# Kernel optimization log

Hardware: AMD Instinct MI355X
Metric: run time of the kernel (lower is better)

## Reference

```python
import jax, jax.numpy as jnp
import numpy as np

SELECT_NUM = 5
N_OBJ = 256


def conv(x, w, b, stride=1, pad=None):
    """NCHW conv. pad=None -> VALID; pad=1 -> [(1,1),(1,1)]."""
    padding = 'VALID' if pad is None else [(pad, pad), (pad, pad)]
    out = jax.lax.conv_general_dilated(
        x, w, (stride, stride), padding,
        dimension_numbers=('NCHW', 'OIHW', 'NCHW'))
    return out + b[None, :, None, None]


def setup_inputs() -> dict:
    key = jax.random.key(0)
    ks = jax.random.split(key, 20)

    def p(k, shape, fan_in):
        return (jax.random.normal(k, shape, jnp.float32) / np.float32(np.sqrt(fan_in)))

    inp = {}
    inp['glob_feature'] = jax.random.normal(ks[0], (1, 1024, 28, 28), jnp.float32)
    inp['roi_features'] = jax.random.normal(ks[1], (N_OBJ, 2048, 7, 7), jnp.float32)
    # valid boxes in a 1280x720 image: x1>x0, y1>y0 so log(.) is finite
    x0 = jax.random.uniform(ks[2], (N_OBJ,), minval=0.0, maxval=600.0)
    y0 = jax.random.uniform(ks[3], (N_OBJ,), minval=0.0, maxval=340.0)
    x1 = x0 + jax.random.uniform(ks[4], (N_OBJ,), minval=10.0, maxval=600.0)
    y1 = y0 + jax.random.uniform(ks[5], (N_OBJ,), minval=10.0, maxval=340.0)
    inp['bbox'] = jnp.stack([x0, y0, x1, y1], axis=1)

    # global branch
    inp['w_glob1'] = p(ks[6], (512, 1024, 4, 4), 1024 * 16); inp['b_glob1'] = jnp.zeros(512, jnp.float32)
    inp['w_glob2'] = p(ks[7], (256, 512, 4, 4), 512 * 16);   inp['b_glob2'] = jnp.zeros(256, jnp.float32)
    # object branch
    inp['w_obj1'] = p(ks[8], (1024, 2048, 3, 3), 2048 * 9);  inp['b_obj1'] = jnp.zeros(1024, jnp.float32)
    inp['w_obj2'] = p(ks[9], (256, 1024, 3, 3), 1024 * 9);   inp['b_obj2'] = jnp.zeros(256, jnp.float32)
    # selector (516 = 260 obj + 256 glob)
    inp['w_sel1'] = p(ks[10], (256, 516, 3, 3), 516 * 9);    inp['b_sel1'] = jnp.zeros(256, jnp.float32)
    inp['w_sel2'] = p(ks[11], (16, 256, 3, 3), 256 * 9);     inp['b_sel2'] = jnp.zeros(16, jnp.float32)
    inp['w_sel3'] = p(ks[12], (1, 16, 3, 3), 16 * 9);        inp['b_sel3'] = jnp.zeros(1, jnp.float32)
    # FC head (eval mode: dropout = identity)
    inp['w_fc1'] = p(ks[13], (516, 256), 516);               inp['b_fc1'] = jnp.zeros(256, jnp.float32)
    inp['w_fc2'] = p(ks[14], (256 * SELECT_NUM, 64), 1280);  inp['b_fc2'] = jnp.zeros(64, jnp.float32)
    inp['w_fc3'] = p(ks[15], (64, 4), 64);                   inp['b_fc3'] = jnp.zeros(4, jnp.float32)
    return inp


def reference(glob_feature, roi_features, bbox,
              w_glob1, b_glob1, w_glob2, b_glob2,
              w_obj1, b_obj1, w_obj2, b_obj2,
              w_sel1, b_sel1, w_sel2, b_sel2, w_sel3, b_sel3,
              w_fc1, b_fc1, w_fc2, b_fc2, w_fc3, b_fc3):
    # global branch: [1,1024,28,28] -> [1,512,14,14] -> [1,256,7,7]; pool(7) is identity
    glob = jax.nn.relu(conv(glob_feature, w_glob1, b_glob1, stride=2, pad=1))
    glob = jax.nn.relu(conv(glob, w_glob2, b_glob2, stride=2, pad=1))

    # object branch: [N,2048,7,7] -> [N,1024,7,7] -> [N,256,7,7]
    obj = jax.nn.relu(conv(roi_features, w_obj1, b_obj1, pad=1))
    obj = jax.nn.relu(conv(obj, w_obj2, b_obj2, pad=1))

    # bbox normalization (uses original coords; image is 1280x720)
    x0, y0, x1, y1 = bbox[:, 0], bbox[:, 1], bbox[:, 2], bbox[:, 3]
    bb = jnp.stack([x0 / 1280.0, y0 / 720.0,
                    jnp.log(1280.0 / (x1 - x0)),
                    jnp.log(720.0 / (y1 - y0))], axis=1)  # [N,4]
    bb = jnp.broadcast_to(bb[:, :, None, None], (bb.shape[0], 4, 7, 7))
    obj = jnp.concatenate([bb, obj], axis=1)  # [N,260,7,7]

    # selector: concat with broadcast glob, 3 valid convs 7->5->3->1
    glob2 = jnp.broadcast_to(glob, (obj.shape[0], 256, 7, 7))
    s = jnp.concatenate([obj, glob2], axis=1)  # [N,516,7,7]
    s = jax.nn.relu(conv(s, w_sel1, b_sel1))
    s = jax.nn.relu(conv(s, w_sel2, b_sel2))
    s = conv(s, w_sel3, b_sel3).reshape(-1)  # [N]

    # top-k selection (sort descending over objects)
    idx = jnp.argsort(-s)[:SELECT_NUM]
    obj = obj[idx] / np.float32(SELECT_NUM)  # [5,260,7,7]

    # adaptive avg pool to 1x1 == mean over HW
    obj = obj.mean(axis=(2, 3))                               # [5,260]
    g = jnp.broadcast_to(glob.mean(axis=(2, 3)), (SELECT_NUM, 256))  # [5,256]
    x = jnp.concatenate([obj, g], axis=1)                     # [5,516]

    x = jax.nn.relu(x @ w_fc1 + b_fc1)   # dropout is identity in eval
    tmp = x.reshape(-1)                  # [1280]
    x = jax.nn.relu(tmp @ w_fc2 + b_fc2) # [64]
    x = x @ w_fc3 + b_fc3                # [4]
    return x
```

## Files before the change

kernel.cpp:

```cpp
#include <hip/hip_runtime.h>
#include <math.h>

using half8 = __attribute__((ext_vector_type(8))) _Float16;
using half4 = __attribute__((ext_vector_type(4))) _Float16;
using f32x4 = __attribute__((ext_vector_type(4))) float;

template<int CIN, int KC, int M_, int BM>
__global__ __launch_bounds__(256)
void transform_w(const float* __restrict__ w, _Float16* __restrict__ wt) {
  constexpr int NT = (KC / 32) * 9;
  __shared__ float lds[32 * 289];
  const int tid = threadIdx.x;
  const int s   = blockIdx.x;
  const int m0  = blockIdx.y * 32;
  const int ci0 = s * 32;
  int vlen = (CIN - ci0) * 9;
  if (vlen > 288) vlen = 288;
  if (vlen < 0) vlen = 0;

  for (int e = tid; e < 32 * 288; e += 256) {
    const int mi = e / 288, o = e - mi * 288;
    float v = 0.f;
    if (o < vlen) v = w[(size_t)(m0 + mi) * (CIN * 9) + (size_t)ci0 * 9 + o];
    lds[mi * 289 + o] = v;
  }
  __syncthreads();

  const int cc  = s >> 2;
  const int sub = s & 3;
  int ns = (KC - 128 * cc) / 32; if (ns > 4) ns = 4;
  const int mt = m0 / BM;
  const int mb = m0 - mt * BM;
  _Float16* base = wt + (size_t)mt * NT * (BM * 32);

  for (int u = tid; u < 36 * 256; u += 256) {
    const int chunk  = u >> 8;
    const int within = u & 255;
    const int g = chunk & 3, khkw = chunk >> 2;
    const int mi = within >> 3, i = within & 7;
    const int kt = 36 * cc + khkw * ns + sub;
    const float v = lds[mi * 289 + (8 * g + i) * 9 + khkw];
    base[(size_t)kt * (BM * 32) + g * (BM * 8) + (mb + mi) * 8 + i] = (_Float16)v;
  }
}

__global__ __launch_bounds__(256)
void convert_tr(const float* __restrict__ x, _Float16* __restrict__ xh) {
  __shared__ _Float16 t_s[49][136];
  const int tid   = threadIdx.x;
  const int cbase = blockIdx.x * 128;
  const int obj   = blockIdx.y;
  const float* src = x + (size_t)obj * 2048 * 49 + (size_t)cbase * 49;
  for (int e = tid; e < 128 * 49; e += 256) {
    const int ci = e / 49, pos = e - ci * 49;
    t_s[pos][ci] = (_Float16)src[e];
  }
  __syncthreads();
  _Float16* dst = xh + (size_t)obj * 49 * 2048 + cbase;
  for (int u = tid; u < 49 * 16; u += 256) {
    const int pos = u >> 4, l = u & 15;
    *(half8*)&dst[(size_t)pos * 2048 + l * 8] = *(const half8*)&t_s[pos][l * 8];
  }
}

template<int KC, int M_, int BM, int FN, int OHW, int PAD, bool TIN, int XROW,
         bool TOUT, typename OUT_T, typename IN_T>
__global__ __launch_bounds__(512, 4)
void conv_mfma(const _Float16* __restrict__ Wt, const IN_T* __restrict__ X,
               const float* __restrict__ bias, OUT_T* __restrict__ out,
               int outc, int co_off) {
  constexpr int NT   = (KC / 32) * 9;
  constexpr int OPOS = OHW * OHW;
  constexpr int WM   = BM / 4;
  constexpr int FR   = WM / 16;

  __shared__ alignas(16) _Float16 x_s[2][50][136];

  const int tid  = threadIdx.x;
  const int wid  = tid >> 6;
  const int lane = tid & 63;
  const int g    = lane >> 4;
  const int ln   = lane & 15;
  const int obj  = wid >> 2;
  const int wm   = (wid & 3) * WM;
  const int mt   = blockIdx.x;
  const int op   = blockIdx.y;

  if (tid < 272) x_s[tid / 136][49][tid % 136] = (_Float16)0.f;

  int ohv[FN], owv[FN];
  bool pvv[FN];
#pragma unroll
  for (int f = 0; f < FN; f++) {
    const int pos = ln + 16 * f;
    pvv[f] = pos < OPOS;
    ohv[f] = pos / OHW;
    owv[f] = pos % OHW;
  }

  f32x4 acc[FR][FN];
#pragma unroll
  for (int r = 0; r < FR; r++)
#pragma unroll
    for (int f = 0; f < FN; f++) acc[r][f] = (f32x4){0.f, 0.f, 0.f, 0.f};

  const _Float16* Xh = nullptr;
  if constexpr (TIN) Xh = (const _Float16*)X + (size_t)(2 * op) * 49 * XROW;

  half8 rg[4];
  auto load_chunk = [&](int cbase, int cw) {
    if (cw == 128) {
#pragma unroll
      for (int v = 0; v < 4; v++) {
        const int u = v * 512 + tid;
        if (u < 1568) {
          const int row = u >> 4, l = u & 15;
          const int o = row >= 49 ? 1 : 0, pos = row - 49 * o;
          rg[v] = *(const half8*)(Xh + (size_t)(o * 49 + pos) * XROW + cbase + l * 8);
        }
      }
    } else {
      if (tid < 392) {
        const int row = tid >> 2, l = tid & 3;
        const int o = row >= 49 ? 1 : 0, pos = row - 49 * o;
        rg[0] = *(const half8*)(Xh + (size_t)(o * 49 + pos) * XROW + cbase + l * 8);
      }
    }
  };
  auto write_chunk = [&](int cw) {
    if (cw == 128) {
#pragma unroll
      for (int v = 0; v < 4; v++) {
        const int u = v * 512 + tid;
        if (u < 1568) {
          const int row = u >> 4, l = u & 15;
          const int o = row >= 49 ? 1 : 0, pos = row - 49 * o;
          *(half8*)&x_s[o][pos][l * 8] = rg[v];
        }
      }
    } else {
      if (tid < 392) {
        const int row = tid >> 2, l = tid & 3;
        const int o = row >= 49 ? 1 : 0, pos = row - 49 * o;
        *(half8*)&x_s[o][pos][l * 8] = rg[0];
      }
    }
  };

  const _Float16* ap = Wt + (size_t)mt * NT * (BM * 32) + (g * BM + wm + ln) * 8;
  half8 afn[FR];
#pragma unroll
  for (int r = 0; r < FR; r++) afn[r] = *(const half8*)(ap + r * 128);

  if constexpr (TIN) load_chunk(0, KC < 128 ? KC : 128);

  for (int cbase = 0; cbase < KC; cbase += 128) {
    const int cw = (KC - cbase < 128) ? (KC - cbase) : 128;
    __syncthreads();
    if constexpr (TIN) {
      write_chunk(cw);
      if (cbase + 128 < KC) {
        const int nw = (KC - cbase - 128 < 128) ? (KC - cbase - 128) : 128;
        load_chunk(cbase + 128, nw);
      }
    } else {
      for (int e = tid; e < 2 * cw * 49; e += 512) {
        const int o = e / (cw * 49);
        const int r = e - o * (cw * 49);
        const int ci = r / 49, pos = r - ci * 49;
        const float v = (float)(X[(size_t)(2 * op + o) * KC * 49 + (size_t)cbase * 49 + r]);
        x_s[o][pos][ci] = (_Float16)v;
      }
    }
    __syncthreads();
    const int nsub = cw / 32;
    for (int khkw = 0; khkw < 9; khkw++) {
      const int kh = khkw / 3, kw = khkw - 3 * (khkw / 3);
      int boff[FN];
#pragma unroll
      for (int f = 0; f < FN; f++) {
        const int ih = ohv[f] + kh - PAD;
        const int iw = owv[f] + kw - PAD;
        bool v = pvv[f];
        if (PAD) v = v && ((unsigned)ih < 7u) && ((unsigned)iw < 7u);
        const int row = v ? (ih * 7 + iw) : 49;
        boff[f] = (obj * 50 * 136 + row * 136) * 2;
      }
      for (int sub = 0; sub < nsub; sub++) {
        half8 af[FR];
#pragma unroll
        for (int r = 0; r < FR; r++) af[r] = afn[r];
        ap += BM * 32;
#pragma unroll
        for (int r = 0; r < FR; r++)
          afn[r] = *(const half8*)(ap + r * 128);
        const char* xb = (const char*)(&x_s[0][0][0]) + (sub * 32 + 8 * g) * 2;
#pragma unroll
        for (int f = 0; f < FN; f++) {
          const half8 bf = *(const half8*)(xb + boff[f]);
#pragma unroll
          for (int r = 0; r < FR; r++)
            acc[r][f] = __builtin_amdgcn_mfma_f32_16x16x32_f16(af[r], bf, acc[r][f], 0, 0, 0);
        }
      }
    }
  }

  const int bo = 2 * op + obj;
#pragma unroll
  for (int f = 0; f < FN; f++) {
    const int pos = ln + 16 * f;
    if (pos < OPOS) {
#pragma unroll
      for (int r = 0; r < FR; r++) {
        const int mrow = mt * BM + wm + r * 16 + g * 4;
        if constexpr (TOUT) {
          half4 h;
#pragma unroll
          for (int e = 0; e < 4; e++)
            h[e] = (_Float16)fmaxf(acc[r][f][e] + bias[mrow + e], 0.f);
          *(half4*)&((_Float16*)out)[((size_t)bo * OPOS + pos) * outc + co_off + mrow] = h;
        } else {
#pragma unroll
          for (int e = 0; e < 4; e++) {
            const int m = mrow + e;
            float v = fmaxf(acc[r][f][e] + bias[m], 0.f);
            out[((size_t)bo * outc + co_off + m) * OPOS + pos] = (OUT_T)v;
          }
        }
      }
    }
  }
}

template<int M_, int CIN, int KH, int KW, int H, int W, int OH, int OW,
         int STRIDE, int PAD, int BATCH, int OUTC, int CO_OFF, bool RELU,
         int TM, int TN, int KSPLIT, bool PARTIAL>
__global__ __launch_bounds__(256)
void conv_gemm(const float* __restrict__ A,
               const float* __restrict__ X,
               const float* __restrict__ bias,
               float* __restrict__ out) {
  constexpr int K   = CIN * KH * KW;
  constexpr int N   = BATCH * OH * OW;
  constexpr int BK  = 16;
  constexpr int BM  = 16 * TM;
  constexpr int BN  = 16 * TN;
  constexpr int KCH = K / KSPLIT;

  __shared__ float a_s[BK][BM];
  __shared__ float b_s[BK][BN];

  const int t  = threadIdx.x;
  const int tx = t & 15;
  const int ty = t >> 4;
  const int n0 = blockIdx.x * BN;
  const int m0 = blockIdx.y * BM;
  const int kz = blockIdx.z;

  constexpr int AQ    = TM / 4;
  constexpr int TPR_A = 4 / AQ;
  const int am = t / TPR_A;
  const int ak = (t % TPR_A) * (4 * AQ);

  constexpr int BQ = TN / 4;
  const int bk = t & 15;
  const int bn = (t >> 4) * TN;

  float acc[TM][TN];
#pragma unroll
  for (int i = 0; i < TM; i++)
#pragma unroll
    for (int j = 0; j < TN; j++) acc[i][j] = 0.f;

  for (int k0 = kz * KCH; k0 < (kz + 1) * KCH; k0 += BK) {
    float4 av[AQ];
#pragma unroll
    for (int q = 0; q < AQ; q++) {
      av[q] = make_float4(0.f, 0.f, 0.f, 0.f);
      const int kq = k0 + ak + 4 * q;
      if ((m0 + am) < M_ && kq < K)
        av[q] = *reinterpret_cast<const float4*>(&A[(m0 + am) * K + kq]);
    }
    float bv[TN];
#pragma unroll
    for (int q = 0; q < TN; q++) bv[q] = 0.f;
    {
      const int kk = k0 + bk;
      if (kk < K) {
        const int ci = kk / (KH * KW);
        const int r  = kk - ci * (KH * KW);
        const int kh = r / KW;
        const int kw = r - kh * KW;
#pragma unroll
        for (int q = 0; q < TN; q++) {
          const int n = n0 + bn + q;
          if (n < N) {
            const int b   = n / (OH * OW);
            const int pos = n - b * (OH * OW);
            const int oh  = pos / OW;
            const int ow  = pos - oh * OW;
            const int ih  = oh * STRIDE - PAD + kh;
            const int iw  = ow * STRIDE - PAD + kw;
            if (ih >= 0 && ih < H && iw >= 0 && iw < W)
              bv[q] = X[((b * CIN + ci) * H + ih) * W + iw];
          }
        }
      }
    }
    __syncthreads();
#pragma unroll
    for (int q = 0; q < AQ; q++) {
      const int kq = ak + 4 * q;
      a_s[kq + 0][am] = av[q].x;
      a_s[kq + 1][am] = av[q].y;
      a_s[kq + 2][am] = av[q].z;
      a_s[kq + 3][am] = av[q].w;
    }
#pragma unroll
    for (int q = 0; q < BQ; q++)
      *reinterpret_cast<float4*>(&b_s[bk][bn + 4 * q]) =
          make_float4(bv[4 * q], bv[4 * q + 1], bv[4 * q + 2], bv[4 * q + 3]);
    __syncthreads();
#pragma unroll
    for (int kk2 = 0; kk2 < BK; kk2++) {
      float a[TM], b[TN];
#pragma unroll
      for (int q = 0; q < AQ; q++)
        *reinterpret_cast<float4*>(&a[4 * q]) =
            *reinterpret_cast<const float4*>(&a_s[kk2][ty * TM + 4 * q]);
#pragma unroll
      for (int q = 0; q < BQ; q++)
        *reinterpret_cast<float4*>(&b[4 * q]) =
            *reinterpret_cast<const float4*>(&b_s[kk2][tx * TN + 4 * q]);
#pragma unroll
      for (int i = 0; i < TM; i++)
#pragma unroll
        for (int j = 0; j < TN; j++)
          acc[i][j] = fmaf(a[i], b[j], acc[i][j]);
    }
  }

#pragma unroll
  for (int i = 0; i < TM; i++) {
    const int m = m0 + ty * TM + i;
    if (m < M_) {
#pragma unroll
      for (int j = 0; j < TN; j++) {
        const int n = n0 + tx * TN + j;
        if (n < N) {
          if (PARTIAL) {
            out[((size_t)kz * M_ + m) * N + n] = acc[i][j];
          } else {
            float v = acc[i][j] + bias[m];
            if (RELU) v = fmaxf(v, 0.f);
            const int b   = n / (OH * OW);
            const int pos = n - b * (OH * OW);
            out[(b * OUTC + CO_OFF + m) * (OH * OW) + pos] = v;
          }
        }
      }
    }
  }
}

__global__ void reduce_bias_relu(const float* __restrict__ part,
                                 const float* __restrict__ bias,
                                 float* __restrict__ out, int MN, int N, int KS) {
  const int e = blockIdx.x * 256 + threadIdx.x;
  if (e >= MN) return;
  float s = 0.f;
  for (int k = 0; k < KS; k++) s += part[(size_t)k * MN + e];
  s += bias[e / N];
  out[e] = fmaxf(s, 0.f);
}

__global__ __launch_bounds__(256)
void sel2_kernel(const float* __restrict__ x, const float* __restrict__ w,
                 const float* __restrict__ b, float* __restrict__ out) {
  const int wv   = (blockIdx.x * 256 + threadIdx.x) >> 6;
  const int lane = threadIdx.x & 63;
  const int obj  = wv >> 4, co = wv & 15;
  float acc[9];
#pragma unroll
  for (int p = 0; p < 9; p++) acc[p] = 0.f;
  const float* xo = x + (size_t)obj * 256 * 25;
  const float* wo = w + (size_t)co * 2304;
  for (int k = lane; k < 2304; k += 64) {
    const int ci = k / 9, rr = k - 9 * ci;
    const int kh = rr / 3, kw = rr - 3 * kh;
    const float wval = wo[k];
    const float* xc = xo + ci * 25;
#pragma unroll
    for (int oh = 0; oh < 3; oh++)
#pragma unroll
      for (int ow = 0; ow < 3; ow++)
        acc[oh * 3 + ow] = fmaf(xc[(oh + kh) * 5 + (ow + kw)], wval, acc[oh * 3 + ow]);
  }
  const float bv = b[co];
#pragma unroll
  for (int p = 0; p < 9; p++) {
    float v = acc[p];
#pragma unroll
    for (int off = 32; off; off >>= 1) v += __shfl_xor(v, off);
    if (lane == 0) out[(size_t)wv * 9 + p] = fmaxf(v + bv, 0.f);
  }
}

__global__ void prep_sin_t(const float* __restrict__ bbox,
                           const float* __restrict__ glob,
                           _Float16* __restrict__ sint) {
  const int b = blockIdx.x;
  const float x0 = bbox[b * 4 + 0], y0 = bbox[b * 4 + 1];
  const float x1 = bbox[b * 4 + 2], y1 = bbox[b * 4 + 3];
  const float bbv[4] = {x0 / 1280.f, y0 / 720.f,
                        logf(1280.f / (x1 - x0)), logf(720.f / (y1 - y0))};
  _Float16* base = sint + (size_t)b * 49 * 544;
  for (int e = threadIdx.x; e < 49 * 288; e += blockDim.x) {
    const int pos = e / 288, q = e - pos * 288;
    float v; int c;
    if (q < 4)        { v = bbv[q];                  c = q; }
    else if (q < 260) { v = glob[(q - 4) * 49 + pos]; c = q + 256; }
    else              { v = 0.f;                      c = q + 256; }
    base[pos * 544 + c] = (_Float16)v;
  }
}

__global__ void score_top5(const float* __restrict__ sel2,
                           const float* __restrict__ w3,
                           const float* __restrict__ b3,
                           int* __restrict__ idx_out) {
  __shared__ float w_s[144];
  __shared__ float s_s[256];
  const int t = threadIdx.x;
  if (t < 144) w_s[t] = w3[t];
  __syncthreads();
  float acc = b3[0];
  const float* p = sel2 + t * 144;
  for (int k = 0; k < 144; k++) acc += p[k] * w_s[k];
  s_s[t] = acc;
  __syncthreads();
  if (t == 0) {
    for (int i = 0; i < 5; i++) {
      float best = -1e30f;
      int bi = 0;
      for (int j = 0; j < 256; j++)
        if (s_s[j] > best) { best = s_s[j]; bi = j; }
      idx_out[i] = bi;
      s_s[bi] = -1e30f;
    }
  }
}

__global__ void pool_t(const _Float16* __restrict__ sint,
                       const float* __restrict__ glob,
                       const int* __restrict__ idx,
                       float* __restrict__ objsel,
                       float* __restrict__ g) {
  const int blk = blockIdx.x;
  const int t = threadIdx.x;
  if (blk < 5) {
    const int b = idx[blk];
    const _Float16* base = sint + (size_t)b * 49 * 544;
    for (int c = t; c < 260; c += blockDim.x) {
      float s = 0.f;
      for (int p = 0; p < 49; p++) s += (float)base[p * 544 + c];
      objsel[blk * 260 + c] = s * (1.f / 245.f);
    }
  } else {
    if (t < 256) {
      float s = 0.f;
      const float* p = glob + t * 49;
      for (int q = 0; q < 49; q++) s += p[q];
      g[t] = s * (1.f / 49.f);
    }
  }
}

__global__ void fc1_kernel(const float* __restrict__ objsel,
                           const float* __restrict__ g,
                           const float* __restrict__ w,
                           const float* __restrict__ b,
                           float* __restrict__ x1) {
  const int co = threadIdx.x;
  float acc[5];
#pragma unroll
  for (int i = 0; i < 5; i++) acc[i] = b[co];
  for (int k = 0; k < 260; k++) {
    const float wv = w[k * 256 + co];
#pragma unroll
    for (int i = 0; i < 5; i++) acc[i] = fmaf(objsel[i * 260 + k], wv, acc[i]);
  }
  for (int k = 260; k < 516; k++) {
    const float wv = w[k * 256 + co];
    const float gv = g[k - 260];
#pragma unroll
    for (int i = 0; i < 5; i++) acc[i] = fmaf(gv, wv, acc[i]);
  }
#pragma unroll
  for (int i = 0; i < 5; i++) x1[i * 256 + co] = fmaxf(acc[i], 0.f);
}

__global__ void fc23_kernel(const float* __restrict__ x1,
                            const float* __restrict__ w2,
                            const float* __restrict__ b2,
                            const float* __restrict__ w3,
                            const float* __restrict__ b3,
                            float* __restrict__ out) {
  __shared__ float x2[64];
  const int j = threadIdx.x;
  float acc = b2[j];
  for (int k = 0; k < 1280; k++) acc = fmaf(x1[k], w2[k * 64 + j], acc);
  x2[j] = fmaxf(acc, 0.f);
  __syncthreads();
  if (j < 4) {
    float a = b3[j];
    for (int k = 0; k < 64; k++) a = fmaf(x2[k], w3[k * 4 + j], a);
    out[j] = a;
  }
}

extern "C" void kernel_launch(void* const* d_in, const int* in_sizes, int n_in,
                              void* d_out, int out_size, void* d_ws, size_t ws_size,
                              hipStream_t stream) {
  (void)in_sizes; (void)n_in; (void)out_size;
  const float* glob_feature = (const float*)d_in[0];
  const float* roi          = (const float*)d_in[1];
  const float* bbox         = (const float*)d_in[2];
  const float* w_glob1      = (const float*)d_in[3];
  const float* b_glob1      = (const float*)d_in[4];
  const float* w_glob2      = (const float*)d_in[5];
  const float* b_glob2      = (const float*)d_in[6];
  const float* w_obj1       = (const float*)d_in[7];
  const float* b_obj1       = (const float*)d_in[8];
  const float* w_obj2       = (const float*)d_in[9];
  const float* b_obj2       = (const float*)d_in[10];
  const float* w_sel1       = (const float*)d_in[11];
  const float* b_sel1       = (const float*)d_in[12];
  const float* w_sel2       = (const float*)d_in[13];
  const float* b_sel2       = (const float*)d_in[14];
  const float* w_sel3       = (const float*)d_in[15];
  const float* b_sel3       = (const float*)d_in[16];
  const float* w_fc1        = (const float*)d_in[17];
  const float* b_fc1        = (const float*)d_in[18];
  const float* w_fc2        = (const float*)d_in[19];
  const float* b_fc2        = (const float*)d_in[20];
  const float* w_fc3        = (const float*)d_in[21];
  const float* b_fc3        = (const float*)d_in[22];

  float* ws = (float*)d_ws;
  const bool big = ws_size >= (size_t)115000000;

  _Float16 *xh1, *wbuf1, *obj1buf, *sint, *wbuf2, *wbufs1;
  float *sel1buf, *glob1buf, *part1, *part2, *sel2buf, *globbuf, *objsel, *gbuf, *x1buf;
  int* idxbuf;

  if (big) {
    xh1      = (_Float16*)(ws);
    wbuf1    = (_Float16*)(ws + 12845056);
    obj1buf  = (_Float16*)(ws + 22282240);
    sint     = (_Float16*)(ws);
    wbuf2    = (_Float16*)(ws + 3411968);
    wbufs1   = (_Float16*)(ws + 4591616);
    sel1buf  = ws + 5218304;
    glob1buf = ws + 6856704;
    part1    = ws + 6957056;
    part2    = ws + 8562688;
    sel2buf  = ws + 8763392;
    globbuf  = ws + 8800256;
    idxbuf   = (int*)(ws + 8812800);
    objsel   = ws + 8812808;
    gbuf     = ws + 8814108;
    x1buf    = ws + 8814364;
  } else {
    xh1      = nullptr;
    wbuf1    = (_Float16*)(ws);
    sint     = (_Float16*)(ws);
    wbuf2    = (_Float16*)(ws + 3412000);
    wbufs1   = (_Float16*)(ws + 4591648);
    sel1buf  = ws + 5218336;
    glob1buf = ws + 6856736;
    part1    = ws + 6957088;
    part2    = ws + 8562720;
    sel2buf  = ws + 8763424;
    obj1buf  = (_Float16*)(ws + 9437184);
    globbuf  = ws + 15859712;
    idxbuf   = (int*)(ws + 15872256);
    objsel   = ws + 15872264;
    gbuf     = ws + 15873564;
    x1buf    = ws + 15873820;
  }

  transform_w<2048, 2048, 1024, 256><<<dim3(64, 32), 256, 0, stream>>>(w_obj1, wbuf1);
  if (big) {
    convert_tr<<<dim3(16, 256), 256, 0, stream>>>(roi, xh1);
    conv_mfma<2048, 1024, 256, 4, 7, 1, true, 2048, true, _Float16, _Float16>
        <<<dim3(4, 128), 512, 0, stream>>>(wbuf1, xh1, b_obj1, obj1buf, 1024, 0);
  } else {
    conv_mfma<2048, 1024, 256, 4, 7, 1, false, 0, true, _Float16, float>
        <<<dim3(4, 128), 512, 0, stream>>>(wbuf1, roi, b_obj1, obj1buf, 1024, 0);
  }

  transform_w<1024, 1024, 256, 128><<<dim3(32, 8), 256, 0, stream>>>(w_obj2, wbuf2);
  transform_w<516, 544, 256, 128><<<dim3(17, 8), 256, 0, stream>>>(w_sel1, wbufs1);

  conv_gemm<512, 1024, 4, 4, 28, 28, 14, 14, 2, 1, 1, 512, 0, true, 4, 4, 16, true>
      <<<dim3(4, 8, 16), 256, 0, stream>>>(w_glob1, glob_feature, b_glob1, part1);
  reduce_bias_relu<<<dim3(392), 256, 0, stream>>>(part1, b_glob1, glob1buf, 100352, 196, 16);
  conv_gemm<256, 512, 4, 4, 14, 14, 7, 7, 2, 1, 1, 256, 0, true, 4, 4, 16, true>
      <<<dim3(1, 4, 16), 256, 0, stream>>>(w_glob2, glob1buf, b_glob2, part2);
  reduce_bias_relu<<<dim3(49), 256, 0, stream>>>(part2, b_glob2, globbuf, 12544, 49, 16);

  prep_sin_t<<<dim3(256), 256, 0, stream>>>(bbox, globbuf, sint);

  conv_mfma<1024, 256, 128, 4, 7, 1, true, 1024, true, _Float16, _Float16>
      <<<dim3(2, 128), 512, 0, stream>>>(wbuf2, obj1buf, b_obj2, sint, 544, 4);
  conv_mfma<544, 256, 128, 2, 5, 0, true, 544, false, float, _Float16>
      <<<dim3(2, 128), 512, 0, stream>>>(wbufs1, sint, b_sel1, sel1buf, 256, 0);
  sel2_kernel<<<dim3(1024), 256, 0, stream>>>(sel1buf, w_sel2, b_sel2, sel2buf);
  score_top5<<<dim3(1), 256, 0, stream>>>(sel2buf, w_sel3, b_sel3, idxbuf);

  pool_t<<<dim3(6), 256, 0, stream>>>(sint, globbuf, idxbuf, objsel, gbuf);
  fc1_kernel<<<dim3(1), 256, 0, stream>>>(objsel, gbuf, w_fc1, b_fc1, x1buf);
  fc23_kernel<<<dim3(1), 64, 0, stream>>>(x1buf, w_fc2, b_fc2, w_fc3, b_fc3,
                                          (float*)d_out);
}
```

Before: 1.154 ms.

## Restructure MFMA conv with triple-buffered weights, block swizzle, LDS-staged output stores

Result: faster. 991.6 us (-14.1%).

```diff
diff --git a/kernel.cpp b/kernel.cpp
--- a/kernel.cpp
+++ b/kernel.cpp
@@ -63,16 +63,19 @@
   }
 }
 
-template<int KC, int M_, int BM, int FN, int OHW, int PAD, bool TIN, int XROW,
-         bool TOUT, typename OUT_T, typename IN_T>
-__global__ __launch_bounds__(512, 4)
-void conv_mfma(const _Float16* __restrict__ Wt, const IN_T* __restrict__ X,
+template<int KC, int BM, int FN, int OHW, int PAD, bool TOUT, typename OUT_T,
+         int NMT, int NOP>
+__global__ __launch_bounds__(512)
+void conv_mfma(const _Float16* __restrict__ Wt, const _Float16* __restrict__ X,
                const float* __restrict__ bias, OUT_T* __restrict__ out,
                int outc, int co_off) {
-  constexpr int NT   = (KC / 32) * 9;
-  constexpr int OPOS = OHW * OHW;
-  constexpr int WM   = BM / 4;
-  constexpr int FR   = WM / 16;
+  constexpr int NT    = (KC / 32) * 9;
+  constexpr int OPOS  = OHW * OHW;
+  constexpr int WM    = BM / 4;
+  constexpr int FR    = WM / 16;
+  constexpr int CFULL = KC / 128;
+  constexpr int TAIL  = KC - CFULL * 128;
+  constexpr int NCH   = CFULL + (TAIL ? 1 : 0);
 
   __shared__ alignas(16) _Float16 x_s[2][50][136];
 
@@ -83,8 +86,12 @@
   const int ln   = lane & 15;
   const int obj  = wid >> 2;
   const int wm   = (wid & 3) * WM;
-  const int mt   = blockIdx.x;
-  const int op   = blockIdx.y;
+
+  const int bid = blockIdx.x;
+  const int j = bid & 7, q = bid >> 3;
+  constexpr int OPJ = 8 / NMT;
+  const int mt = j / OPJ;
+  const int op = (j % OPJ) * (NOP / OPJ) + q;
 
   if (tid < 272) x_s[tid / 136][49][tid % 136] = (_Float16)0.f;
 
@@ -104,8 +111,7 @@
 #pragma unroll
     for (int f = 0; f < FN; f++) acc[r][f] = (f32x4){0.f, 0.f, 0.f, 0.f};
 
-  const _Float16* Xh = nullptr;
-  if constexpr (TIN) Xh = (const _Float16*)X + (size_t)(2 * op) * 49 * XROW;
+  const _Float16* Xh = X + (size_t)(2 * op) * 49 * KC;
 
   half8 rg[4];
   auto load_chunk = [&](int cbase, int cw) {
@@ -116,14 +122,14 @@
         if (u < 1568) {
           const int row = u >> 4, l = u & 15;
           const int o = row >= 49 ? 1 : 0, pos = row - 49 * o;
-          rg[v] = *(const half8*)(Xh + (size_t)(o * 49 + pos) * XROW + cbase + l * 8);
+          rg[v] = *(const half8*)(Xh + (size_t)(o * 49 + pos) * KC + cbase + l * 8);
         }
       }
     } else {
       if (tid < 392) {
         const int row = tid >> 2, l = tid & 3;
         const int o = row >= 49 ? 1 : 0, pos = row - 49 * o;
-        rg[0] = *(const half8*)(Xh + (size_t)(o * 49 + pos) * XROW + cbase + l * 8);
+        rg[0] = *(const half8*)(Xh + (size_t)(o * 49 + pos) * KC + cbase + l * 8);
       }
     }
   };
@@ -147,80 +153,132 @@
     }
   };
 
-  const _Float16* ap = Wt + (size_t)mt * NT * (BM * 32) + (g * BM + wm + ln) * 8;
-  half8 afn[FR];
-#pragma unroll
-  for (int r = 0; r < FR; r++) afn[r] = *(const half8*)(ap + r * 128);
-
-  if constexpr (TIN) load_chunk(0, KC < 128 ? KC : 128);
-
-  for (int cbase = 0; cbase < KC; cbase += 128) {
-    const int cw = (KC - cbase < 128) ? (KC - cbase) : 128;
-    __syncthreads();
-    if constexpr (TIN) {
-      write_chunk(cw);
-      if (cbase + 128 < KC) {
-        const int nw = (KC - cbase - 128 < 128) ? (KC - cbase - 128) : 128;
-        load_chunk(cbase + 128, nw);
+  const int afoff = (g * BM + wm + ln) * 8;
+  const _Float16* ap = Wt + (size_t)mt * NT * (BM * 32) + afoff;
+  half8 afA[FR], afB[FR], afC[FR];
+#pragma unroll
+  for (int r = 0; r < FR; r++) afA[r] = *(const half8*)(ap + r * 128);
+  ap += BM * 32;
+#pragma unroll
+  for (int r = 0; r < FR; r++) afB[r] = *(const half8*)(ap + r * 128);
+  ap += BM * 32;
+
+  load_chunk(0, KC < 128 ? KC : 128);
+
+  auto kstep = [&](half8 (&cur)[FR], half8 (&fut)[FR], int subbyte,
+                   const int (&boff)[FN]) {
+#pragma unroll
+    for (int r = 0; r < FR; r++) fut[r] = *(const half8*)(ap + r * 128);
+    ap += BM * 32;
+    __builtin_amdgcn_s_setprio(1);
+    const char* xb = (const char*)(&x_s[0][0][0]) + subbyte;
+#pragma unroll
+    for (int f = 0; f < FN; f++) {
+      const half8 bf = *(const half8*)(xb + boff[f]);
+#pragma unroll
+      for (int r = 0; r < FR; r++)
+        acc[r][f] = __builtin_amdgcn_mfma_f32_16x16x32_f16(cur[r], bf, acc[r][f], 0, 0, 0);
+    }
+    __builtin_amdgcn_s_setprio(0);
+  };
+
+  for (int c = 0; c < NCH; c++) {
+    const int cw = (c < CFULL) ? 128 : TAIL;
+    asm volatile("s_barrier" ::: "memory");
+    write_chunk(cw);
+    if (c + 1 < NCH)
+      load_chunk((c + 1) * 128, (c + 1 < CFULL) ? 128 : TAIL);
+    asm volatile("s_waitcnt lgkmcnt(0)\n\ts_barrier" ::: "memory");
+
+    if (cw == 128) {
+#pragma unroll
+      for (int t9 = 0; t9 < 9; t9++) {
+        const int kh = t9 / 3, kw = t9 - 3 * (t9 / 3);
+        int boff[FN];
+#pragma unroll
+        for (int f = 0; f < FN; f++) {
+          const int ih = ohv[f] + kh - PAD;
+          const int iw = owv[f] + kw - PAD;
+          bool v = pvv[f];
+          if (PAD) v = v && ((unsigned)ih < 7u) && ((unsigned)iw < 7u);
+          const int row = v ? (ih * 7 + iw) : 49;
+          boff[f] = (obj * 50 * 136 + row * 136) * 2;
+        }
+#pragma unroll
+        for (int s4 = 0; s4 < 4; s4++) {
+          const int ph = (t9 * 4 + s4) % 3;
+          const int subbyte = (s4 * 32 + 8 * g) * 2;
+          if (ph == 0)      kstep(afA, afC, subbyte, boff);
+          else if (ph == 1) kstep(afB, afA, subbyte, boff);
+          else              kstep(afC, afB, subbyte, boff);
+        }
       }
     } else {
-      for (int e = tid; e < 2 * cw * 49; e += 512) {
-        const int o = e / (cw * 49);
-        const int r = e - o * (cw * 49);
-        const int ci = r / 49, pos = r - ci * 49;
-        const float v = (float)(X[(size_t)(2 * op + o) * KC * 49 + (size_t)cbase * 49 + r]);
-        x_s[o][pos][ci] = (_Float16)v;
-      }
-    }
-    __syncthreads();
-    const int nsub = cw / 32;
-    for (int khkw = 0; khkw < 9; khkw++) {
-      const int kh = khkw / 3, kw = khkw - 3 * (khkw / 3);
-      int boff[FN];
-#pragma unroll
-      for (int f = 0; f < FN; f++) {
-        const int ih = ohv[f] + kh - PAD;
-        const int iw = owv[f] + kw - PAD;
-        bool v = pvv[f];
-        if (PAD) v = v && ((unsigned)ih < 7u) && ((unsigned)iw < 7u);
-        const int row = v ? (ih * 7 + iw) : 49;
-        boff[f] = (obj * 50 * 136 + row * 136) * 2;
-      }
-      for (int sub = 0; sub < nsub; sub++) {
-        half8 af[FR];
-#pragma unroll
-        for (int r = 0; r < FR; r++) af[r] = afn[r];
-        ap += BM * 32;
-#pragma unroll
-        for (int r = 0; r < FR; r++)
-          afn[r] = *(const half8*)(ap + r * 128);
-        const char* xb = (const char*)(&x_s[0][0][0]) + (sub * 32 + 8 * g) * 2;
+#pragma unroll
+      for (int t9 = 0; t9 < 9; t9++) {
+        const int kh = t9 / 3, kw = t9 - 3 * (t9 / 3);
+        int boff[FN];
 #pragma unroll
         for (int f = 0; f < FN; f++) {
-          const half8 bf = *(const half8*)(xb + boff[f]);
-#pragma unroll
-          for (int r = 0; r < FR; r++)
-            acc[r][f] = __builtin_amdgcn_mfma_f32_16x16x32_f16(af[r], bf, acc[r][f], 0, 0, 0);
-        }
-      }
-    }
-  }
-
-  const int bo = 2 * op + obj;
-#pragma unroll
-  for (int f = 0; f < FN; f++) {
-    const int pos = ln + 16 * f;
-    if (pos < OPOS) {
-#pragma unroll
-      for (int r = 0; r < FR; r++) {
-        const int mrow = mt * BM + wm + r * 16 + g * 4;
-        if constexpr (TOUT) {
-          half4 h;
-#pragma unroll
-          for (int e = 0; e < 4; e++)
-            h[e] = (_Float16)fmaxf(acc[r][f][e] + bias[mrow + e], 0.f);
-          *(half4*)&((_Float16*)out)[((size_t)bo * OPOS + pos) * outc + co_off + mrow] = h;
-        } else {
+          const int ih = ohv[f] + kh - PAD;
+          const int iw = owv[f] + kw - PAD;
+          bool v = pvv[f];
+          if (PAD) v = v && ((unsigned)ih < 7u) && ((unsigned)iw < 7u);
+          const int row = v ? (ih * 7 + iw) : 49;
+          boff[f] = (obj * 50 * 136 + row * 136) * 2;
+        }
+        const int ph = t9 % 3;
+        const int subbyte = (8 * g) * 2;
+        if (ph == 0)      kstep(afA, afC, subbyte, boff);
+        else if (ph == 1) kstep(afB, afA, subbyte, boff);
+        else              kstep(afC, afB, subbyte, boff);
+      }
+    }
+  }
+
+  if constexpr (TOUT) {
+    __shared__ alignas(16) _Float16 ot_s[2][49][132];
+    constexpr int PASSES = BM / 128;
+#pragma unroll
+    for (int p = 0; p < PASSES; p++) {
+      if (p) asm volatile("s_barrier" ::: "memory");
+      if (wm >= 128 * p && wm < 128 * (p + 1)) {
+#pragma unroll
+        for (int f = 0; f < FN; f++) {
+          const int pos = ln + 16 * f;
+          if (pos < OPOS) {
+#pragma unroll
+            for (int r = 0; r < FR; r++) {
+              const int cl = wm - 128 * p + r * 16 + g * 4;
+              half4 h;
+#pragma unroll
+              for (int e = 0; e < 4; e++)
+                h[e] = (_Float16)fmaxf(
+                    acc[r][f][e] + bias[mt * BM + wm + r * 16 + g * 4 + e], 0.f);
+              *(half4*)&ot_s[obj][pos][cl] = h;
+            }
+          }
+        }
+      }
+      asm volatile("s_waitcnt lgkmcnt(0)\n\ts_barrier" ::: "memory");
+      _Float16* dst = (_Float16*)out;
+      for (int u = tid; u < 2 * 49 * 32; u += 512) {
+        const int row = u >> 5, l = u & 31;
+        const int o = row >= 49 ? 1 : 0, pos = row - 49 * o;
+        const half4 v = *(const half4*)&ot_s[o][pos][l * 4];
+        *(half4*)&dst[((size_t)(2 * op + o) * OPOS + pos) * outc +
+                      co_off + mt * BM + 128 * p + l * 4] = v;
+      }
+    }
+  } else {
+    const int bo = 2 * op + obj;
+#pragma unroll
+    for (int f = 0; f < FN; f++) {
+      const int pos = ln + 16 * f;
+      if (pos < OPOS) {
+#pragma unroll
+        for (int r = 0; r < FR; r++) {
+          const int mrow = mt * BM + wm + r * 16 + g * 4;
 #pragma unroll
           for (int e = 0; e < 4; e++) {
             const int m = mrow + e;
@@ -523,7 +581,7 @@
 extern "C" void kernel_launch(void* const* d_in, const int* in_sizes, int n_in,
                               void* d_out, int out_size, void* d_ws, size_t ws_size,
                               hipStream_t stream) {
-  (void)in_sizes; (void)n_in; (void)out_size;
+  (void)in_sizes; (void)n_in; (void)out_size; (void)ws_size;
   const float* glob_feature = (const float*)d_in[0];
   const float* roi          = (const float*)d_in[1];
   const float* bbox         = (const float*)d_in[2];
@@ -549,57 +607,27 @@
   const float* b_fc3        = (const float*)d_in[22];
 
   float* ws = (float*)d_ws;
-  const bool big = ws_size >= (size_t)115000000;
-
-  _Float16 *xh1, *wbuf1, *obj1buf, *sint, *wbuf2, *wbufs1;
-  float *sel1buf, *glob1buf, *part1, *part2, *sel2buf, *globbuf, *objsel, *gbuf, *x1buf;
-  int* idxbuf;
-
-  if (big) {
-    xh1      = (_Float16*)(ws);
-    wbuf1    = (_Float16*)(ws + 12845056);
-    obj1buf  = (_Float16*)(ws + 22282240);
-    sint     = (_Float16*)(ws);
-    wbuf2    = (_Float16*)(ws + 3411968);
-    wbufs1   = (_Float16*)(ws + 4591616);
-    sel1buf  = ws + 5218304;
-    glob1buf = ws + 6856704;
-    part1    = ws + 6957056;
-    part2    = ws + 8562688;
-    sel2buf  = ws + 8763392;
-    globbuf  = ws + 8800256;
-    idxbuf   = (int*)(ws + 8812800);
-    objsel   = ws + 8812808;
-    gbuf     = ws + 8814108;
-    x1buf    = ws + 8814364;
-  } else {
-    xh1      = nullptr;
-    wbuf1    = (_Float16*)(ws);
-    sint     = (_Float16*)(ws);
-    wbuf2    = (_Float16*)(ws + 3412000);
-    wbufs1   = (_Float16*)(ws + 4591648);
-    sel1buf  = ws + 5218336;
-    glob1buf = ws + 6856736;
-    part1    = ws + 6957088;
-    part2    = ws + 8562720;
-    sel2buf  = ws + 8763424;
-    obj1buf  = (_Float16*)(ws + 9437184);
-    globbuf  = ws + 15859712;
-    idxbuf   = (int*)(ws + 15872256);
-    objsel   = ws + 15872264;
-    gbuf     = ws + 15873564;
-    x1buf    = ws + 15873820;
-  }
+  _Float16* xh1     = (_Float16*)(ws);
+  _Float16* wbuf1   = (_Float16*)(ws + 12845056);
+  _Float16* obj1buf = (_Float16*)(ws + 22282240);
+  _Float16* sint    = (_Float16*)(ws);
+  _Float16* wbuf2   = (_Float16*)(ws + 3411968);
+  _Float16* wbufs1  = (_Float16*)(ws + 4591616);
+  float*    sel1buf = ws + 5218304;
+  float*    glob1buf= ws + 6856704;
+  float*    part1   = ws + 6957056;
+  float*    part2   = ws + 8562688;
+  float*    sel2buf = ws + 8763392;
+  float*    globbuf = ws + 8800256;
+  int*      idxbuf  = (int*)(ws + 8812800);
+  float*    objsel  = ws + 8812808;
+  float*    gbuf    = ws + 8814108;
+  float*    x1buf   = ws + 8814364;
 
   transform_w<2048, 2048, 1024, 256><<<dim3(64, 32), 256, 0, stream>>>(w_obj1, wbuf1);
-  if (big) {
-    convert_tr<<<dim3(16, 256), 256, 0, stream>>>(roi, xh1);
-    conv_mfma<2048, 1024, 256, 4, 7, 1, true, 2048, true, _Float16, _Float16>
-        <<<dim3(4, 128), 512, 0, stream>>>(wbuf1, xh1, b_obj1, obj1buf, 1024, 0);
-  } else {
-    conv_mfma<2048, 1024, 256, 4, 7, 1, false, 0, true, _Float16, float>
-        <<<dim3(4, 128), 512, 0, stream>>>(wbuf1, roi, b_obj1, obj1buf, 1024, 0);
-  }
+  convert_tr<<<dim3(16, 256), 256, 0, stream>>>(roi, xh1);
+  conv_mfma<2048, 256, 4, 7, 1, true, _Float16, 4, 128>
+      <<<dim3(512), 512, 0, stream>>>(wbuf1, xh1, b_obj1, obj1buf, 1024, 0);
 
   transform_w<1024, 1024, 256, 128><<<dim3(32, 8), 256, 0, stream>>>(w_obj2, wbuf2);
   transform_w<516, 544, 256, 128><<<dim3(17, 8), 256, 0, stream>>>(w_sel1, wbufs1);
@@ -613,10 +641,10 @@
 
   prep_sin_t<<<dim3(256), 256, 0, stream>>>(bbox, globbuf, sint);
 
-  conv_mfma<1024, 256, 128, 4, 7, 1, true, 1024, true, _Float16, _Float16>
-      <<<dim3(2, 128), 512, 0, stream>>>(wbuf2, obj1buf, b_obj2, sint, 544, 4);
-  conv_mfma<544, 256, 128, 2, 5, 0, true, 544, false, float, _Float16>
-      <<<dim3(2, 128), 512, 0, stream>>>(wbufs1, sint, b_sel1, sel1buf, 256, 0);
+  conv_mfma<1024, 128, 4, 7, 1, true, _Float16, 2, 128>
+      <<<dim3(256), 512, 0, stream>>>(wbuf2, obj1buf, b_obj2, sint, 544, 4);
+  conv_mfma<544, 128, 2, 5, 0, false, float, 2, 128>
+      <<<dim3(256), 512, 0, stream>>>(wbufs1, sint, b_sel1, sel1buf, 256, 0);
   sel2_kernel<<<dim3(1024), 256, 0, stream>>>(sel1buf, w_sel2, b_sel2, sel2buf);
   score_top5<<<dim3(1), 256, 0, stream>>>(sel2buf, w_sel3, b_sel3, idxbuf);
 
```
